# Kernel tuning notes

Hardware: AMD Instinct MI355X
Metric: run time of the kernel (lower is better)

The kernel has to match this reference:

```python
import jax, jax.numpy as jnp
import numpy as np
import math

B, N, D, KA, H = 8, 1024, 512, 16, 8
QD = D // 4
HD = D // H


def qsplit(x):
    q = x.shape[-1] // 4
    return x[..., :q], x[..., q:2*q], x[..., 2*q:3*q], x[..., 3*q:]


def hprod(p, q):
    pr, pi, pj, pk = qsplit(p)
    qr, qi, qj, qk = qsplit(q)
    return jnp.concatenate([
        pr*qr - pi*qi - pj*qj - pk*qk,
        pr*qi + pi*qr + pj*qk - pk*qj,
        pr*qj - pi*qk + pj*qr + pk*qi,
        pr*qk + pi*qj - pj*qi + pk*qr,
    ], axis=-1)


def qconj(x):
    r, i, j, k = qsplit(x)
    return jnp.concatenate([r, -i, -j, -k], axis=-1)


def qlin(x, w, b):
    # w: [4, qo, qi] -> Hamilton block matrix [4qo, 4qi]
    r, i, j, k = w[0], w[1], w[2], w[3]
    W = jnp.concatenate([
        jnp.concatenate([r, -i, -j, -k], axis=1),
        jnp.concatenate([i,  r, -k,  j], axis=1),
        jnp.concatenate([j,  k,  r, -i], axis=1),
        jnp.concatenate([k, -j,  i,  r], axis=1),
    ], axis=0)
    return x @ W.T + b


def qln(x, gamma, beta):
    # per-component LayerNorm over Q; gamma/beta: [4, Q]
    qd = x.shape[-1] // 4
    xs = x.reshape(x.shape[:-1] + (4, qd))
    m = xs.mean(-1, keepdims=True)
    v = xs.var(-1, keepdims=True)
    y = (xs - m) / jnp.sqrt(v + 1e-5) * gamma + beta
    return y.reshape(x.shape)


def setup_inputs():
    key = jax.random.key(0)
    ks = jax.random.split(key, 20)
    lim = math.sqrt(6.0 / (2 * QD))  # xavier for [QD, QD]
    def qw(k):
        return jax.random.uniform(k, (4, QD, QD), minval=-lim, maxval=lim)
    return {
        'q': jax.random.normal(ks[0], (B, N, D), dtype=jnp.float32),
        'spike': jax.random.uniform(ks[1], (B, N), dtype=jnp.float32),
        'mask': jnp.ones((B, N), dtype=jnp.float32),
        'theta_logit': jnp.float32(0.0),
        'w_prim': qw(ks[2]), 'b_prim': jnp.zeros((D,), jnp.float32),
        'anchors': jax.random.normal(ks[3], (KA, D)) * 0.5,
        'log_sigma': jnp.zeros((KA,), jnp.float32),
        'w_aggr': qw(ks[4]), 'b_aggr': jnp.zeros((D,), jnp.float32),
        'w_q': qw(ks[5]), 'b_q': jnp.zeros((D,), jnp.float32),
        'w_k': qw(ks[6]), 'b_k': jnp.zeros((D,), jnp.float32),
        'w_v': qw(ks[7]), 'b_v': jnp.zeros((D,), jnp.float32),
        'w_o': qw(ks[8]), 'b_o': jnp.zeros((D,), jnp.float32),
        'ln_gamma': jnp.ones((4, QD), jnp.float32),
        'ln_beta': jnp.zeros((4, QD), jnp.float32),
    }


def reference(q, spike, mask, theta_logit, w_prim, b_prim, anchors, log_sigma,
              w_aggr, b_aggr, w_q, b_q, w_k, b_k, w_v, b_v, w_o, b_o,
              ln_gamma, ln_beta):
    b, n, d = q.shape
    qd = d // 4
    # --- SpikeQuaternionRotation: rotate toward K-axis by theta = theta_max*spike ---
    theta_max = (jnp.pi / 2) * jax.nn.sigmoid(theta_logit)
    theta = theta_max * spike                      # [B, N]
    c = jnp.cos(theta)[..., None]
    s = jnp.sin(theta)[..., None]
    z = jnp.zeros_like(c)
    rot = jnp.concatenate([
        jnp.broadcast_to(c, (b, n, qd)),
        jnp.broadcast_to(z, (b, n, qd)),
        jnp.broadcast_to(z, (b, n, qd)),
        jnp.broadcast_to(s, (b, n, qd)),
    ], axis=-1)
    q_rot = hprod(rot, q)                          # [B, N, D]

    # --- PrimaryLayer: per-cell quaternion transform ---
    msg_p = qlin(q_rot, w_prim, b_prim)

    # --- QuaternionAnchorLayer ---
    a_conj = qconj(anchors)                        # [KA, D]
    prod = hprod(q_rot[:, None, :, :], a_conj[None, :, None, :])  # [B, KA, N, D]
    dist = jnp.sum(prod * prod, axis=-1)           # [B, KA, N]
    sigma_sq = jnp.maximum(jnp.exp(log_sigma) ** 2, 1e-6)
    incid = jnp.exp(-dist / sigma_sq[None, :, None]) * mask[:, None, :]
    denom = jnp.maximum(incid.sum(-1, keepdims=True), 1e-6)
    h = jnp.einsum('bkn,bnd->bkd', incid, q_rot) / denom  # [B, KA, D]
    h = qlin(h, w_aggr, b_aggr)

    # --- QuaternionMHA(query=q_rot, key=h, value=h), no mask ---
    Qh = qlin(q_rot, w_q, b_q).reshape(b, n, H, HD)
    Kh = qlin(h, w_k, b_k).reshape(b, KA, H, HD)
    Vh = qlin(h, w_v, b_v).reshape(b, KA, H, HD)
    scores = jnp.einsum('bqhd,bkhd->bhqk', Qh, Kh) / jnp.sqrt(jnp.float32(HD))
    attn = jax.nn.softmax(scores, axis=-1)
    out = jnp.einsum('bhqk,bkhd->bqhd', attn, Vh).reshape(b, n, d)
    msg_a = qlin(out, w_o, b_o)

    # --- residual + per-component LayerNorm ---
    return qln(q + msg_p + msg_a, ln_gamma, ln_beta)
```

## Files before the change

### kernel.cpp

```cpp
#include <hip/hip_runtime.h>
#include <hip/hip_bf16.h>

typedef __hip_bfloat16 bf16;
typedef __attribute__((ext_vector_type(8))) short bf16x8;
typedef __attribute__((ext_vector_type(4))) float f32x4;

__device__ __forceinline__ float bflo(unsigned u) { return __uint_as_float(u << 16); }
__device__ __forceinline__ float bfhi(unsigned u) { return __uint_as_float(u & 0xffff0000u); }
__device__ __forceinline__ bool probe_f32(const void* mask) {
  return *(const unsigned*)mask == 0x3F800000u;
}
__device__ __forceinline__ float ldin(const void* p, size_t i, bool f32) {
  return f32 ? ((const float*)p)[i] : (float)((const bf16*)p)[i];
}

__global__ __launch_bounds__(256) void prologue(
    const void* w0, const void* w1, const void* w2, const void* w3,
    const void* w4, const void* w5,
    const void* b0, const void* b1, const void* b2, const void* b3,
    const void* b4, const void* b5, const void* g, const void* be,
    const void* q, const void* spike, const void* theta_logit, const void* mask,
    bf16* __restrict__ Wall, float* __restrict__ biasF,
    bf16* __restrict__ q_rot, float* __restrict__ qn) {
  bool f32 = probe_f32(mask);
  int blk = blockIdx.x, t = threadIdx.x;
  if (blk < 1536) {
    const int compT[4][4] = {{0,1,2,3},{1,0,3,2},{2,3,0,1},{3,2,1,0}};
    const float signT[4][4] = {{1.f,-1.f,-1.f,-1.f},{1.f,1.f,-1.f,1.f},{1.f,1.f,1.f,-1.f},{1.f,-1.f,1.f,1.f}};
    int E = blk * 1024 + t * 4;
    int wi = E >> 18;
    const void* src = wi == 0 ? w0 : wi == 1 ? w1 : wi == 2 ? w2 : wi == 3 ? w3 : wi == 4 ? w4 : w5;
    bf16 ov[4];
    #pragma unroll
    for (int j = 0; j < 4; ++j) {
      int e = (E + j) & 262143;
      int o = e >> 9, kk = e & 511;
      int ro = o >> 7, a = o & 127, co = kk >> 7, b2 = kk & 127;
      ov[j] = (bf16)(ldin(src, compT[ro][co] * 16384 + a * 128 + b2, f32) * signT[ro][co]);
    }
    *(uint2*)(Wall + E) = *(const uint2*)ov;
  } else if (blk < 1544) {
    int b = blk - 1536;
    const void* src = b == 0 ? b0 : b == 1 ? b1 : b == 2 ? b2 : b == 3 ? b3
                    : b == 4 ? b4 : b == 5 ? b5 : b == 6 ? g : be;
    biasF[b * 512 + t] = ldin(src, t, f32);
    biasF[b * 512 + 256 + t] = ldin(src, 256 + t, f32);
  } else {
    int row = (blk - 1544) * 2 + (t >> 7);
    int l = t & 127;
    float tl = ldin(theta_logit, 0, f32);
    float tmax = 1.5707963267948966f / (1.0f + __expf(-tl));
    float th = tmax * ldin(spike, row, f32);
    float c = cosf(th), s = sinf(th);
    size_t base = (size_t)row * 512;
    float a = ldin(q, base + l, f32), b = ldin(q, base + 128 + l, f32);
    float cc = ldin(q, base + 256 + l, f32), d = ldin(q, base + 384 + l, f32);
    float r0 = c * a - s * d;
    float r1 = c * b - s * cc;
    float r2 = c * cc + s * b;
    float r3 = c * d + s * a;
    bf16* orow = q_rot + base;
    orow[l] = (bf16)r0; orow[128 + l] = (bf16)r1; orow[256 + l] = (bf16)r2; orow[384 + l] = (bf16)r3;
    qn[(size_t)row * 128 + l] = r0 * r0 + r1 * r1 + r2 * r2 + r3 * r3;
  }
}

__device__ __forceinline__ void stage_B64(const bf16* __restrict__ Bw, int n0, char* Bs, int t) {
  int r = t & 63, cb = (t >> 6) * 16;
  const bf16* src = Bw + (size_t)(n0 + r) * 512;
  #pragma unroll
  for (int i = 0; i < 16; ++i) {
    int c = cb + i;
    int off = (c >> 2) * 4096 + (r >> 4) * 1024 + (((c & 3) * 16 + (r & 15)) * 16);
    *(uint4*)(Bs + off) = *(const uint4*)(src + c * 8);
  }
}

__global__ __launch_bounds__(256, 2) void gemm1(
    const bf16* __restrict__ A, const bf16* __restrict__ Bw,
    const float* __restrict__ bias0, const float* __restrict__ bias1,
    bf16* __restrict__ MQ) {
  __shared__ char Bs[65536];
  const int t = threadIdx.x;
  const int wave = t >> 6, lane = t & 63;
  const int quad = lane >> 4, l16 = lane & 15;
  const int m0 = blockIdx.x * 256, n0 = blockIdx.y * 64;
  stage_B64(Bw, n0, Bs, t);
  __syncthreads();
  const int mbase = m0 + wave * 64;
  f32x4 acc[4][4] = {};
  bf16x8 areg[2][4], breg[2][4];
  #pragma unroll
  for (int mt = 0; mt < 4; ++mt)
    areg[0][mt] = *(const bf16x8*)(A + (size_t)(mbase + mt * 16 + l16) * 512 + quad * 8);
  #pragma unroll
  for (int nt = 0; nt < 4; ++nt)
    breg[0][nt] = *(const bf16x8*)(Bs + nt * 1024 + lane * 16);
  #pragma unroll
  for (int kk = 0; kk < 16; ++kk) {
    const int cur = kk & 1, nxt = cur ^ 1;
    if (kk < 15) {
      const int k2 = (kk + 1) * 32;
      #pragma unroll
      for (int mt = 0; mt < 4; ++mt)
        areg[nxt][mt] = *(const bf16x8*)(A + (size_t)(mbase + mt * 16 + l16) * 512 + k2 + quad * 8);
      #pragma unroll
      for (int nt = 0; nt < 4; ++nt)
        breg[nxt][nt] = *(const bf16x8*)(Bs + (kk + 1) * 4096 + nt * 1024 + lane * 16);
    }
    #pragma unroll
    for (int mt = 0; mt < 4; ++mt)
      #pragma unroll
      for (int nt = 0; nt < 4; ++nt)
        acc[mt][nt] = __builtin_amdgcn_mfma_f32_16x16x32_bf16(areg[cur][mt], breg[cur][nt],
                                                              acc[mt][nt], 0, 0, 0);
  }
  #pragma unroll
  for (int nt = 0; nt < 4; ++nt) {
    int col = n0 + nt * 16 + l16;
    float bv = col < 512 ? bias0[col] : bias1[col - 512];
    #pragma unroll
    for (int mt = 0; mt < 4; ++mt) {
      int rb = mbase + mt * 16 + quad * 4;
      #pragma unroll
      for (int r = 0; r < 4; ++r)
        MQ[(size_t)(rb + r) * 1024 + col] = (bf16)(acc[mt][nt][r] + bv);
    }
  }
}

__global__ __launch_bounds__(256, 2) void gemm2(
    const bf16* __restrict__ A, const bf16* __restrict__ Bw,
    const float* __restrict__ biasO, bf16* __restrict__ msg_a) {
  __shared__ char Bs[65536];
  const int t = threadIdx.x;
  const int wave = t >> 6, lane = t & 63;
  const int quad = lane >> 4, l16 = lane & 15;
  const int m0 = blockIdx.x * 128, n0 = blockIdx.y * 64;
  stage_B64(Bw, n0, Bs, t);
  __syncthreads();
  const int mbase = m0 + wave * 32;
  f32x4 acc[2][4] = {};
  bf16x8 areg[2][2], breg[2][4];
  #pragma unroll
  for (int mt = 0; mt < 2; ++mt)
    areg[0][mt] = *(const bf16x8*)(A + (size_t)(mbase + mt * 16 + l16) * 512 + quad * 8);
  #pragma unroll
  for (int nt = 0; nt < 4; ++nt)
    breg[0][nt] = *(const bf16x8*)(Bs + nt * 1024 + lane * 16);
  #pragma unroll
  for (int kk = 0; kk < 16; ++kk) {
    const int cur = kk & 1, nxt = cur ^ 1;
    if (kk < 15) {
      const int k2 = (kk + 1) * 32;
      #pragma unroll
      for (int mt = 0; mt < 2; ++mt)
        areg[nxt][mt] = *(const bf16x8*)(A + (size_t)(mbase + mt * 16 + l16) * 512 + k2 + quad * 8);
      #pragma unroll
      for (int nt = 0; nt < 4; ++nt)
        breg[nxt][nt] = *(const bf16x8*)(Bs + (kk + 1) * 4096 + nt * 1024 + lane * 16);
    }
    #pragma unroll
    for (int mt = 0; mt < 2; ++mt)
      #pragma unroll
      for (int nt = 0; nt < 4; ++nt)
        acc[mt][nt] = __builtin_amdgcn_mfma_f32_16x16x32_bf16(areg[cur][mt], breg[cur][nt],
                                                              acc[mt][nt], 0, 0, 0);
  }
  #pragma unroll
  for (int nt = 0; nt < 4; ++nt) {
    int col = n0 + nt * 16 + l16;
    float bv = biasO[col];
    #pragma unroll
    for (int mt = 0; mt < 2; ++mt) {
      int rb = mbase + mt * 16 + quad * 4;
      #pragma unroll
      for (int r = 0; r < 4; ++r)
        msg_a[(size_t)(rb + r) * 512 + col] = (bf16)(acc[mt][nt][r] + bv);
    }
  }
}

__global__ __launch_bounds__(256) void dist_h(
    const float* __restrict__ qn, const bf16* __restrict__ q_rot,
    const void* anchors, const void* lsig, const void* mask,
    float* __restrict__ h_raw, float* __restrict__ denom) {
  bool f32 = probe_f32(mask);
  __shared__ bf16 qr[64 * 512];
  __shared__ float an[16 * 128];
  __shared__ float sInc[16 * 64];
  __shared__ float rs[16];
  __shared__ float pd[16];
  int b = blockIdx.x, nc = blockIdx.y;
  int t = threadIdx.x;
  {
    const uint4* src = (const uint4*)(q_rot + ((size_t)b * 1024 + nc * 64) * 512);
    uint4* dst = (uint4*)qr;
    #pragma unroll
    for (int i = 0; i < 8; ++i) dst[t + i * 256] = src[t + i * 256];
  }
  for (int i = t; i < 2048; i += 256) {
    int k = i >> 7, l = i & 127;
    float a0 = ldin(anchors, k * 512 + l, f32);
    float a1 = ldin(anchors, k * 512 + 128 + l, f32);
    float a2 = ldin(anchors, k * 512 + 256 + l, f32);
    float a3 = ldin(anchors, k * 512 + 384 + l, f32);
    an[i] = a0 * a0 + a1 * a1 + a2 * a2 + a3 * a3;
  }
  if (t < 16) {
    float ls = ldin(lsig, t, f32);
    float ssq = __expf(ls); ssq = fmaxf(ssq * ssq, 1e-6f);
    rs[t] = -1.0f / ssq;
    pd[t] = 0.0f;
  }
  __syncthreads();
  {
    int rl = t >> 2, part = t & 3;
    int n = nc * 64 + rl;
    const float* qrow = qn + ((size_t)b * 1024 + n) * 128 + part * 32;
    f32x4 q4[8];
    #pragma unroll
    for (int i = 0; i < 8; ++i) q4[i] = *(const f32x4*)(qrow + i * 4);
    float sc[16] = {};
    #pragma unroll
    for (int i = 0; i < 8; ++i) {
      #pragma unroll
      for (int k = 0; k < 16; ++k) {
        f32x4 av = *(const f32x4*)(an + k * 128 + part * 32 + i * 4);
        sc[k] += q4[i][0] * av[0] + q4[i][1] * av[1] + q4[i][2] * av[2] + q4[i][3] * av[3];
      }
    }
    #pragma unroll
    for (int k = 0; k < 16; ++k) {
      sc[k] += __shfl_xor(sc[k], 1, 64);
      sc[k] += __shfl_xor(sc[k], 2, 64);
    }
    if (part == 0) {
      float mval = ldin(mask, b * 1024 + n, f32);
      float lsum = 0.0f;
      #pragma unroll
      for (int k = 0; k < 16; ++k) {
        float inc = __expf(sc[k] * rs[k]) * mval;
        sInc[k * 64 + rl] = inc;
        lsum += inc;
      }
      #pragma unroll
      for (int k = 0; k < 16; ++k) atomicAdd(&pd[k], sInc[k * 64 + rl]);
      (void)lsum;
    }
  }
  __syncthreads();
  {
    float acc0[16] = {}, acc1[16] = {};
    for (int nn = 0; nn < 64; ++nn) {
      float v0 = (float)qr[nn * 512 + t];
      float v1 = (float)qr[nn * 512 + 256 + t];
      #pragma unroll
      for (int k = 0; k < 16; ++k) {
        float p = sInc[k * 64 + nn];
        acc0[k] += p * v0;
        acc1[k] += p * v1;
      }
    }
    #pragma unroll
    for (int k = 0; k < 16; ++k) {
      atomicAdd(&h_raw[((size_t)(b * 16 + k)) * 512 + t], acc0[k]);
      atomicAdd(&h_raw[((size_t)(b * 16 + k)) * 512 + 256 + t], acc1[k]);
    }
  }
  if (t < 16) atomicAdd(&denom[b * 16 + t], pd[t]);
}

__global__ void qlin_aggr(const float* __restrict__ X, const float* __restrict__ denom,
                          const bf16* __restrict__ W, const float* __restrict__ bias,
                          float* __restrict__ Y) {
  __shared__ float xs[512];
  int row = blockIdx.x, half = blockIdx.y;
  int t = threadIdx.x;
  float dinv = 1.0f / fmaxf(denom[row], 1e-6f);
  xs[t] = X[(size_t)row * 512 + t] * dinv;
  xs[256 + t] = X[(size_t)row * 512 + 256 + t] * dinv;
  __syncthreads();
  int o = half * 256 + t;
  const uint4* wr = (const uint4*)(W + (size_t)o * 512);
  float acc = bias[o];
  #pragma unroll 4
  for (int c = 0; c < 64; ++c) {
    uint4 u = wr[c];
    const float* xp = xs + c * 8;
    acc += xp[0] * bflo(u.x) + xp[1] * bfhi(u.x)
         + xp[2] * bflo(u.y) + xp[3] * bfhi(u.y)
         + xp[4] * bflo(u.z) + xp[5] * bfhi(u.z)
         + xp[6] * bflo(u.w) + xp[7] * bfhi(u.w);
  }
  Y[(size_t)row * 512 + o] = acc;
}

__global__ void qlin_kv(const float* __restrict__ X,
                        const bf16* __restrict__ Wk, const float* __restrict__ bk,
                        const bf16* __restrict__ Wv, const float* __restrict__ bv,
                        float* __restrict__ Kh, float* __restrict__ Vh) {
  __shared__ float xs[512];
  int row = blockIdx.x, half = blockIdx.y;
  int t = threadIdx.x;
  xs[t] = X[(size_t)row * 512 + t];
  xs[256 + t] = X[(size_t)row * 512 + 256 + t];
  __syncthreads();
  int o = half * 256 + t;
  const uint4* wk = (const uint4*)(Wk + (size_t)o * 512);
  const uint4* wv = (const uint4*)(Wv + (size_t)o * 512);
  float ak = bk[o], av = bv[o];
  #pragma unroll 2
  for (int c = 0; c < 64; ++c) {
    uint4 uk = wk[c], uv = wv[c];
    const float* xp = xs + c * 8;
    ak += xp[0] * bflo(uk.x) + xp[1] * bfhi(uk.x)
        + xp[2] * bflo(uk.y) + xp[3] * bfhi(uk.y)
        + xp[4] * bflo(uk.z) + xp[5] * bfhi(uk.z)
        + xp[6] * bflo(uk.w) + xp[7] * bfhi(uk.w);
    av += xp[0] * bflo(uv.x) + xp[1] * bfhi(uv.x)
        + xp[2] * bflo(uv.y) + xp[3] * bfhi(uv.y)
        + xp[4] * bflo(uv.z) + xp[5] * bfhi(uv.z)
        + xp[6] * bflo(uv.w) + xp[7] * bfhi(uv.w);
  }
  Kh[(size_t)row * 512 + o] = ak;
  Vh[(size_t)row * 512 + o] = av;
}

__global__ __launch_bounds__(256) void attn_v3(
    const bf16* __restrict__ MQ, const float* __restrict__ Kh_g,
    const float* __restrict__ Vh_g, bf16* __restrict__ attn_o) {
  __shared__ float KV[8 * 1092];
  __shared__ float P[16 * 132];
  const int t = threadIdx.x;
  const int rowbase = blockIdx.x * 16;
  const int b = rowbase >> 10;
  for (int i = t; i < 8192; i += 256) {
    int k = i >> 9, d = i & 511, h = d >> 6, dd = d & 63;
    KV[h * 1092 + k * 68 + dd] = Kh_g[(size_t)b * 8192 + i];
  }
  __syncthreads();
  if (t < 128) {
    const int r = t >> 3, h = t & 7;
    const int grow = rowbase + r;
    const uint4* qp = (const uint4*)(MQ + (size_t)grow * 1024 + 512 + h * 64);
    float q[64];
    #pragma unroll
    for (int i = 0; i < 8; ++i) {
      uint4 u = qp[i];
      q[i * 8 + 0] = bflo(u.x); q[i * 8 + 1] = bfhi(u.x);
      q[i * 8 + 2] = bflo(u.y); q[i * 8 + 3] = bfhi(u.y);
      q[i * 8 + 4] = bflo(u.z); q[i * 8 + 5] = bfhi(u.z);
      q[i * 8 + 6] = bflo(u.w); q[i * 8 + 7] = bfhi(u.w);
    }
    float sc[16];
    #pragma unroll
    for (int k = 0; k < 16; ++k) {
      float s = 0.0f;
      #pragma unroll
      for (int d4 = 0; d4 < 16; ++d4) {
        f32x4 kv = *(const f32x4*)(KV + h * 1092 + k * 68 + d4 * 4);
        s += q[d4 * 4 + 0] * kv[0] + q[d4 * 4 + 1] * kv[1]
           + q[d4 * 4 + 2] * kv[2] + q[d4 * 4 + 3] * kv[3];
      }
      sc[k] = s * 0.125f;
    }
    float m = sc[0];
    #pragma unroll
    for (int k = 1; k < 16; ++k) m = fmaxf(m, sc[k]);
    float ssum = 0.0f;
    #pragma unroll
    for (int k = 0; k < 16; ++k) { sc[k] = __expf(sc[k] - m); ssum += sc[k]; }
    float inv = 1.0f / ssum;
    #pragma unroll
    for (int k = 0; k < 16; ++k) P[r * 132 + h * 16 + k] = sc[k] * inv;
  }
  __syncthreads();
  for (int i = t; i < 8192; i += 256) {
    int k = i >> 9, d = i & 511, h = d >> 6, dd = d & 63;
    KV[h * 1092 + k * 68 + dd] = Vh_g[(size_t)b * 8192 + i];
  }
  __syncthreads();
  {
    const int r = t >> 4, dg = t & 15;
    #pragma unroll
    for (int h = 0; h < 8; ++h) {
      float a0 = 0, a1 = 0, a2 = 0, a3 = 0;
      #pragma unroll
      for (int k = 0; k < 16; ++k) {
        float p = P[r * 132 + h * 16 + k];
        f32x4 va = *(const f32x4*)(KV + h * 1092 + k * 68 + dg * 4);
        a0 += p * va[0]; a1 += p * va[1]; a2 += p * va[2]; a3 += p * va[3];
      }
      bf16 ov[4] = {(bf16)a0, (bf16)a1, (bf16)a2, (bf16)a3};
      *(uint2*)(attn_o + (size_t)(rowbase + r) * 512 + h * 64 + dg * 4) = *(const uint2*)ov;
    }
  }
}

__global__ __launch_bounds__(256) void ln_v2(
    const void* q, const void* mask, const bf16* __restrict__ MQ,
    const bf16* __restrict__ msg_a, const float* __restrict__ gamF, void* out) {
  bool f32 = probe_f32(mask);
  int t = threadIdx.x;
  int row = blockIdx.x * 2 + (t >> 7);
  int l = t & 127;
  int e0 = l * 4;
  float x[4];
  {
    uint2 um = *(const uint2*)(MQ + (size_t)row * 1024 + e0);
    uint2 ua = *(const uint2*)(msg_a + (size_t)row * 512 + e0);
    float qv[4];
    if (f32) {
      f32x4 qq = *(const f32x4*)((const float*)q + (size_t)row * 512 + e0);
      qv[0] = qq[0]; qv[1] = qq[1]; qv[2] = qq[2]; qv[3] = qq[3];
    } else {
      uint2 uq = *(const uint2*)((const bf16*)q + (size_t)row * 512 + e0);
      qv[0] = bflo(uq.x); qv[1] = bfhi(uq.x); qv[2] = bflo(uq.y); qv[3] = bfhi(uq.y);
    }
    x[0] = qv[0] + bflo(um.x) + bflo(ua.x);
    x[1] = qv[1] + bfhi(um.x) + bfhi(ua.x);
    x[2] = qv[2] + bflo(um.y) + bflo(ua.y);
    x[3] = qv[3] + bfhi(um.y) + bfhi(ua.y);
  }
  float s = x[0] + x[1] + x[2] + x[3];
  float s2 = x[0] * x[0] + x[1] * x[1] + x[2] * x[2] + x[3] * x[3];
  #pragma unroll
  for (int off = 1; off <= 16; off <<= 1) {
    s  += __shfl_xor(s, off, 64);
    s2 += __shfl_xor(s2, off, 64);
  }
  float m = s * (1.0f / 128.0f);
  float rinv = rsqrtf(s2 * (1.0f / 128.0f) - m * m + 1e-5f);
  f32x4 ga = *(const f32x4*)(gamF + e0);
  f32x4 be = *(const f32x4*)(gamF + 512 + e0);
  float y[4];
  #pragma unroll
  for (int j = 0; j < 4; ++j) y[j] = (x[j] - m) * rinv * ga[j] + be[j];
  if (f32) {
    f32x4 ov = {y[0], y[1], y[2], y[3]};
    *(f32x4*)((float*)out + (size_t)row * 512 + e0) = ov;
  } else {
    bf16 ov[4] = {(bf16)y[0], (bf16)y[1], (bf16)y[2], (bf16)y[3]};
    *(uint2*)((bf16*)out + (size_t)row * 512 + e0) = *(const uint2*)ov;
  }
}

extern "C" void kernel_launch(void* const* d_in, const int* in_sizes, int n_in,
                              void* d_out, int out_size, void* d_ws, size_t ws_size,
                              hipStream_t stream) {
  (void)in_sizes; (void)n_in; (void)out_size; (void)ws_size;
  const void* q      = d_in[0];
  const void* spike  = d_in[1];
  const void* mask   = d_in[2];
  const void* tl     = d_in[3];
  const void* w_prim = d_in[4];
  const void* b_prim = d_in[5];
  const void* anchors= d_in[6];
  const void* lsig   = d_in[7];
  const void* w_aggr = d_in[8];
  const void* b_aggr = d_in[9];
  const void* w_q    = d_in[10];
  const void* b_q    = d_in[11];
  const void* w_k    = d_in[12];
  const void* b_k    = d_in[13];
  const void* w_v    = d_in[14];
  const void* b_v    = d_in[15];
  const void* w_o    = d_in[16];
  const void* b_o    = d_in[17];
  const void* gam    = d_in[18];
  const void* bet    = d_in[19];

  char* ws = (char*)d_ws;
  bf16*  Wall   = (bf16*)(ws + 0);
  bf16*  q_rot  = (bf16*)(ws + 3145728);
  float* qn     = (float*)(ws + 11534336);
  bf16*  MQ     = (bf16*)(ws + 15728640);
  float* h_raw  = (float*)(ws + 32505856);
  float* denom  = (float*)(ws + 32768000);
  float* h2     = (float*)(ws + 32770048);
  float* Kh     = (float*)(ws + 33032192);
  float* Vh     = (float*)(ws + 33294336);
  bf16*  attn_o = (bf16*)(ws + 33556480);
  bf16*  msg_a  = (bf16*)(ws + 41945088);
  float* biasF  = (float*)(ws + 50333696);

  hipMemsetAsync(h_raw, 0, 262144 + 2048, stream);
  prologue<<<5640, 256, 0, stream>>>(w_prim, w_q, w_o, w_aggr, w_k, w_v,
                                     b_prim, b_q, b_o, b_aggr, b_k, b_v, gam, bet,
                                     q, spike, tl, mask, Wall, biasF, q_rot, qn);
  gemm1<<<dim3(32, 16), 256, 0, stream>>>(q_rot, Wall, biasF + 0, biasF + 512, MQ);
  dist_h<<<dim3(8, 16), 256, 0, stream>>>(qn, q_rot, anchors, lsig, mask, h_raw, denom);
  qlin_aggr<<<dim3(128, 2), 256, 0, stream>>>(h_raw, denom, Wall + 3 * 262144, biasF + 1536, h2);
  qlin_kv<<<dim3(128, 2), 256, 0, stream>>>(h2, Wall + 4 * 262144, biasF + 2048,
                                            Wall + 5 * 262144, biasF + 2560, Kh, Vh);
  attn_v3<<<512, 256, 0, stream>>>(MQ, Kh, Vh, attn_o);
  gemm2<<<dim3(64, 8), 256, 0, stream>>>(attn_o, Wall + 2 * 262144, biasF + 1024, msg_a);
  ln_v2<<<4096, 256, 0, stream>>>(q, mask, MQ, msg_a, biasF + 3072, d_out);
}
```

Before: 230.3 us.

## Replace global atomics with partial buffers, fuse aggr/KV qlins, split attn scores

```diff
diff --git a/kernel.cpp b/kernel.cpp
--- a/kernel.cpp
+++ b/kernel.cpp
@@ -184,7 +184,7 @@
 __global__ __launch_bounds__(256) void dist_h(
     const float* __restrict__ qn, const bf16* __restrict__ q_rot,
     const void* anchors, const void* lsig, const void* mask,
-    float* __restrict__ h_raw, float* __restrict__ denom) {
+    float* __restrict__ h_part, float* __restrict__ pd_part) {
   bool f32 = probe_f32(mask);
   __shared__ bf16 qr[64 * 512];
   __shared__ float an[16 * 128];
@@ -237,16 +237,12 @@
     }
     if (part == 0) {
       float mval = ldin(mask, b * 1024 + n, f32);
-      float lsum = 0.0f;
       #pragma unroll
       for (int k = 0; k < 16; ++k) {
         float inc = __expf(sc[k] * rs[k]) * mval;
         sInc[k * 64 + rl] = inc;
-        lsum += inc;
+        atomicAdd(&pd[k], inc);
       }
-      #pragma unroll
-      for (int k = 0; k < 16; ++k) atomicAdd(&pd[k], sInc[k * 64 + rl]);
-      (void)lsum;
     }
   }
   __syncthreads();
@@ -264,67 +260,68 @@
     }
     #pragma unroll
     for (int k = 0; k < 16; ++k) {
-      atomicAdd(&h_raw[((size_t)(b * 16 + k)) * 512 + t], acc0[k]);
-      atomicAdd(&h_raw[((size_t)(b * 16 + k)) * 512 + 256 + t], acc1[k]);
-    }
-  }
-  if (t < 16) atomicAdd(&denom[b * 16 + t], pd[t]);
-}
-
-__global__ void qlin_aggr(const float* __restrict__ X, const float* __restrict__ denom,
-                          const bf16* __restrict__ W, const float* __restrict__ bias,
-                          float* __restrict__ Y) {
+      size_t base = ((size_t)(b * 16 + k) * 16 + nc) * 512;
+      h_part[base + t] = acc0[k];
+      h_part[base + 256 + t] = acc1[k];
+    }
+  }
+  if (t < 16) pd_part[((size_t)(b * 16 + t)) * 16 + nc] = pd[t];
+}
+
+__global__ __launch_bounds__(512) void qlin_hkv(
+    const float* __restrict__ h_part, const float* __restrict__ pd_part,
+    const bf16* __restrict__ Wa, const float* __restrict__ ba,
+    const bf16* __restrict__ Wk, const float* __restrict__ bk,
+    const bf16* __restrict__ Wv, const float* __restrict__ bv,
+    float* __restrict__ Kh, float* __restrict__ Vh) {
   __shared__ float xs[512];
-  int row = blockIdx.x, half = blockIdx.y;
+  __shared__ float ys[512];
+  int row = blockIdx.x;
   int t = threadIdx.x;
-  float dinv = 1.0f / fmaxf(denom[row], 1e-6f);
-  xs[t] = X[(size_t)row * 512 + t] * dinv;
-  xs[256 + t] = X[(size_t)row * 512 + 256 + t] * dinv;
-  __syncthreads();
-  int o = half * 256 + t;
-  const uint4* wr = (const uint4*)(W + (size_t)o * 512);
-  float acc = bias[o];
-  #pragma unroll 4
-  for (int c = 0; c < 64; ++c) {
-    uint4 u = wr[c];
-    const float* xp = xs + c * 8;
-    acc += xp[0] * bflo(u.x) + xp[1] * bfhi(u.x)
-         + xp[2] * bflo(u.y) + xp[3] * bfhi(u.y)
-         + xp[4] * bflo(u.z) + xp[5] * bfhi(u.z)
-         + xp[6] * bflo(u.w) + xp[7] * bfhi(u.w);
-  }
-  Y[(size_t)row * 512 + o] = acc;
-}
-
-__global__ void qlin_kv(const float* __restrict__ X,
-                        const bf16* __restrict__ Wk, const float* __restrict__ bk,
-                        const bf16* __restrict__ Wv, const float* __restrict__ bv,
-                        float* __restrict__ Kh, float* __restrict__ Vh) {
-  __shared__ float xs[512];
-  int row = blockIdx.x, half = blockIdx.y;
-  int t = threadIdx.x;
-  xs[t] = X[(size_t)row * 512 + t];
-  xs[256 + t] = X[(size_t)row * 512 + 256 + t];
-  __syncthreads();
-  int o = half * 256 + t;
-  const uint4* wk = (const uint4*)(Wk + (size_t)o * 512);
-  const uint4* wv = (const uint4*)(Wv + (size_t)o * 512);
-  float ak = bk[o], av = bv[o];
-  #pragma unroll 2
-  for (int c = 0; c < 64; ++c) {
-    uint4 uk = wk[c], uv = wv[c];
-    const float* xp = xs + c * 8;
-    ak += xp[0] * bflo(uk.x) + xp[1] * bfhi(uk.x)
-        + xp[2] * bflo(uk.y) + xp[3] * bfhi(uk.y)
-        + xp[4] * bflo(uk.z) + xp[5] * bfhi(uk.z)
-        + xp[6] * bflo(uk.w) + xp[7] * bfhi(uk.w);
-    av += xp[0] * bflo(uv.x) + xp[1] * bfhi(uv.x)
-        + xp[2] * bflo(uv.y) + xp[3] * bfhi(uv.y)
-        + xp[4] * bflo(uv.z) + xp[5] * bfhi(uv.z)
-        + xp[6] * bflo(uv.w) + xp[7] * bfhi(uv.w);
-  }
-  Kh[(size_t)row * 512 + o] = ak;
-  Vh[(size_t)row * 512 + o] = av;
+  float dsum = 0.0f;
+  #pragma unroll
+  for (int nc = 0; nc < 16; ++nc) dsum += pd_part[row * 16 + nc];
+  float dinv = 1.0f / fmaxf(dsum, 1e-6f);
+  float hv = 0.0f;
+  #pragma unroll
+  for (int nc = 0; nc < 16; ++nc) hv += h_part[(size_t)row * 8192 + nc * 512 + t];
+  xs[t] = hv * dinv;
+  __syncthreads();
+  {
+    const uint4* wr = (const uint4*)(Wa + (size_t)t * 512);
+    float acc = ba[t];
+    #pragma unroll 4
+    for (int c = 0; c < 64; ++c) {
+      uint4 u = wr[c];
+      const float* xp = xs + c * 8;
+      acc += xp[0] * bflo(u.x) + xp[1] * bfhi(u.x)
+           + xp[2] * bflo(u.y) + xp[3] * bfhi(u.y)
+           + xp[4] * bflo(u.z) + xp[5] * bfhi(u.z)
+           + xp[6] * bflo(u.w) + xp[7] * bfhi(u.w);
+    }
+    ys[t] = acc;
+  }
+  __syncthreads();
+  {
+    const uint4* wk = (const uint4*)(Wk + (size_t)t * 512);
+    const uint4* wv = (const uint4*)(Wv + (size_t)t * 512);
+    float ak = bk[t], av = bv[t];
+    #pragma unroll 2
+    for (int c = 0; c < 64; ++c) {
+      uint4 uk = wk[c], uv = wv[c];
+      const float* xp = ys + c * 8;
+      ak += xp[0] * bflo(uk.x) + xp[1] * bfhi(uk.x)
+          + xp[2] * bflo(uk.y) + xp[3] * bfhi(uk.y)
+          + xp[4] * bflo(uk.z) + xp[5] * bfhi(uk.z)
+          + xp[6] * bflo(uk.w) + xp[7] * bfhi(uk.w);
+      av += xp[0] * bflo(uv.x) + xp[1] * bfhi(uv.x)
+          + xp[2] * bflo(uv.y) + xp[3] * bfhi(uv.y)
+          + xp[4] * bflo(uv.z) + xp[5] * bfhi(uv.z)
+          + xp[6] * bflo(uv.w) + xp[7] * bfhi(uv.w);
+    }
+    Kh[(size_t)row * 512 + t] = ak;
+    Vh[(size_t)row * 512 + t] = av;
+  }
 }
 
 __global__ __launch_bounds__(256) void attn_v3(
@@ -340,13 +337,13 @@
     KV[h * 1092 + k * 68 + dd] = Kh_g[(size_t)b * 8192 + i];
   }
   __syncthreads();
-  if (t < 128) {
-    const int r = t >> 3, h = t & 7;
+  {
+    const int r = t >> 4, h = (t >> 1) & 7, hf = t & 1;
     const int grow = rowbase + r;
-    const uint4* qp = (const uint4*)(MQ + (size_t)grow * 1024 + 512 + h * 64);
-    float q[64];
-    #pragma unroll
-    for (int i = 0; i < 8; ++i) {
+    const uint4* qp = (const uint4*)(MQ + (size_t)grow * 1024 + 512 + h * 64 + hf * 32);
+    float q[32];
+    #pragma unroll
+    for (int i = 0; i < 4; ++i) {
       uint4 u = qp[i];
       q[i * 8 + 0] = bflo(u.x); q[i * 8 + 1] = bfhi(u.x);
       q[i * 8 + 2] = bflo(u.y); q[i * 8 + 3] = bfhi(u.y);
@@ -358,22 +355,28 @@
     for (int k = 0; k < 16; ++k) {
       float s = 0.0f;
       #pragma unroll
-      for (int d4 = 0; d4 < 16; ++d4) {
-        f32x4 kv = *(const f32x4*)(KV + h * 1092 + k * 68 + d4 * 4);
+      for (int d4 = 0; d4 < 8; ++d4) {
+        f32x4 kv = *(const f32x4*)(KV + h * 1092 + k * 68 + hf * 32 + d4 * 4);
         s += q[d4 * 4 + 0] * kv[0] + q[d4 * 4 + 1] * kv[1]
            + q[d4 * 4 + 2] * kv[2] + q[d4 * 4 + 3] * kv[3];
       }
-      sc[k] = s * 0.125f;
-    }
-    float m = sc[0];
-    #pragma unroll
-    for (int k = 1; k < 16; ++k) m = fmaxf(m, sc[k]);
-    float ssum = 0.0f;
-    #pragma unroll
-    for (int k = 0; k < 16; ++k) { sc[k] = __expf(sc[k] - m); ssum += sc[k]; }
-    float inv = 1.0f / ssum;
-    #pragma unroll
-    for (int k = 0; k < 16; ++k) P[r * 132 + h * 16 + k] = sc[k] * inv;
+      sc[k] = s;
+    }
+    #pragma unroll
+    for (int k = 0; k < 16; ++k) sc[k] += __shfl_xor(sc[k], 1, 64);
+    if (hf == 0) {
+      #pragma unroll
+      for (int k = 0; k < 16; ++k) sc[k] *= 0.125f;
+      float m = sc[0];
+      #pragma unroll
+      for (int k = 1; k < 16; ++k) m = fmaxf(m, sc[k]);
+      float ssum = 0.0f;
+      #pragma unroll
+      for (int k = 0; k < 16; ++k) { sc[k] = __expf(sc[k] - m); ssum += sc[k]; }
+      float inv = 1.0f / ssum;
+      #pragma unroll
+      for (int k = 0; k < 16; ++k) P[r * 132 + h * 16 + k] = sc[k] * inv;
+    }
   }
   __syncthreads();
   for (int i = t; i < 8192; i += 256) {
@@ -476,24 +479,23 @@
   bf16*  q_rot  = (bf16*)(ws + 3145728);
   float* qn     = (float*)(ws + 11534336);
   bf16*  MQ     = (bf16*)(ws + 15728640);
-  float* h_raw  = (float*)(ws + 32505856);
-  float* denom  = (float*)(ws + 32768000);
-  float* h2     = (float*)(ws + 32770048);
-  float* Kh     = (float*)(ws + 33032192);
-  float* Vh     = (float*)(ws + 33294336);
-  bf16*  attn_o = (bf16*)(ws + 33556480);
-  bf16*  msg_a  = (bf16*)(ws + 41945088);
-  float* biasF  = (float*)(ws + 50333696);
-
-  hipMemsetAsync(h_raw, 0, 262144 + 2048, stream);
+  float* h_part = (float*)(ws + 32505856);
+  float* pd_part= (float*)(ws + 36700160);
+  float* Kh     = (float*)(ws + 36708352);
+  float* Vh     = (float*)(ws + 36970496);
+  bf16*  attn_o = (bf16*)(ws + 37232640);
+  bf16*  msg_a  = (bf16*)(ws + 45621248);
+  float* biasF  = (float*)(ws + 54009856);
+
   prologue<<<5640, 256, 0, stream>>>(w_prim, w_q, w_o, w_aggr, w_k, w_v,
                                      b_prim, b_q, b_o, b_aggr, b_k, b_v, gam, bet,
                                      q, spike, tl, mask, Wall, biasF, q_rot, qn);
   gemm1<<<dim3(32, 16), 256, 0, stream>>>(q_rot, Wall, biasF + 0, biasF + 512, MQ);
-  dist_h<<<dim3(8, 16), 256, 0, stream>>>(qn, q_rot, anchors, lsig, mask, h_raw, denom);
-  qlin_aggr<<<dim3(128, 2), 256, 0, stream>>>(h_raw, denom, Wall + 3 * 262144, biasF + 1536, h2);
-  qlin_kv<<<dim3(128, 2), 256, 0, stream>>>(h2, Wall + 4 * 262144, biasF + 2048,
-                                            Wall + 5 * 262144, biasF + 2560, Kh, Vh);
+  dist_h<<<dim3(8, 16), 256, 0, stream>>>(qn, q_rot, anchors, lsig, mask, h_part, pd_part);
+  qlin_hkv<<<128, 512, 0, stream>>>(h_part, pd_part,
+                                    Wall + 3 * 262144, biasF + 1536,
+                                    Wall + 4 * 262144, biasF + 2048,
+                                    Wall + 5 * 262144, biasF + 2560, Kh, Vh);
   attn_v3<<<512, 256, 0, stream>>>(MQ, Kh, Vh, attn_o);
   gemm2<<<dim3(64, 8), 256, 0, stream>>>(attn_o, Wall + 2 * 262144, biasF + 1024, msg_a);
   ln_v2<<<4096, 256, 0, stream>>>(q, mask, MQ, msg_a, biasF + 3072, d_out);
```

Result: slower. 244.0 us (+6.0%).
